# Performance work log

Measured on AMD Instinct MI355X. Metric: run time of the kernel, lower is better.

The kernel has to match this reference:

```python
import jax, jax.numpy as jnp
import numpy as np

LABEL_LEN = 48
PRED_LEN = 96
D_MODEL = 512


def _pos_embed(L, d):
    pos = np.arange(L, dtype=np.float32)[:, None]
    div = np.exp(np.arange(0, d, 2, dtype=np.float32) * (-np.log(10000.0) / d))
    pe = np.zeros((L, d), np.float32)
    pe[:, 0::2] = np.sin(pos * div)
    pe[:, 1::2] = np.cos(pos * div)
    return jnp.asarray(pe)


def _embed(x, conv_w):
    # x: [B, L, C]; circular conv1d k=3 (TokenEmbedding) + sinusoidal PE
    xp = jnp.pad(jnp.transpose(x, (0, 2, 1)), ((0, 0), (0, 0), (1, 1)), mode='wrap')
    y = jax.lax.conv_general_dilated(xp, conv_w, (1,), 'VALID',
                                     dimension_numbers=('NCH', 'OIH', 'NCH'))
    y = jnp.transpose(y, (0, 2, 1))  # [B, L, D]
    return y + _pos_embed(y.shape[1], y.shape[2])


def _lstm_cell(x, h, c, Wih, Whh, b):
    g = x @ Wih.T + h @ Whh.T + b
    i, f, gg, o = jnp.split(g, 4, axis=-1)  # torch gate order i,f,g,o
    c = jax.nn.sigmoid(f) * c + jax.nn.sigmoid(i) * jnp.tanh(gg)
    h = jax.nn.sigmoid(o) * jnp.tanh(c)
    return h, c


def _lstm(xs, Wih, Whh, b):
    B, _, _ = xs.shape
    H = Whh.shape[1]
    init = (jnp.zeros((B, H), xs.dtype), jnp.zeros((B, H), xs.dtype))
    def step(carry, x):
        h, c = _lstm_cell(x, carry[0], carry[1], Wih, Whh, b)
        return (h, c), h
    (h, c), ys = jax.lax.scan(step, init, jnp.transpose(xs, (1, 0, 2)))
    return jnp.transpose(ys, (1, 0, 2)), h, c


def _forward(x_enc, x_dec, emb_enc_w, emb_dec_w, enc_Wih, enc_Whh, enc_b,
             dec_Wih, dec_Whh, dec_b, attn_W, attn_b, v, fc_W, fc_b,
             proj_W, proj_b):
    H = D_MODEL
    enc_in = _embed(x_enc, emb_enc_w)                 # [B, Le, H]
    dec_in = _embed(x_dec, emb_dec_w)                 # [B, Ld, H]
    enc_out, h0, c0 = _lstm(enc_in, enc_Wih, enc_Whh, enc_b)  # [B, Le, H]

    # precompute encoder part of Bahdanau score: attn(cat(h, enc)) splits columnwise
    Wh, We = attn_W[:, :H], attn_W[:, H:]
    enc_part = jnp.einsum('blh,kh->blk', enc_out, We) + attn_b   # [B, Le, H]
    # precompute input gates for decoded timesteps
    xs = dec_in[:, LABEL_LEN:PRED_LEN, :]                         # [B, T, H]
    xg = jnp.einsum('bth,gh->btg', xs, dec_Wih) + dec_b           # [B, T, 4H]

    def step(carry, xg_t):
        h, c = carry
        g = xg_t + h @ dec_Whh.T
        i, f, gg, o = jnp.split(g, 4, axis=-1)
        c = jax.nn.sigmoid(f) * c + jax.nn.sigmoid(i) * jnp.tanh(gg)
        h = jax.nn.sigmoid(o) * jnp.tanh(c)
        feat = jnp.tanh(enc_part + (h @ Wh.T)[:, None, :])        # [B, Le, H]
        scores = feat @ v                                          # [B, Le]
        aw = jax.nn.softmax(scores, axis=1)
        ctx = jnp.einsum('bl,blh->bh', aw, enc_out)                # [B, H]
        out = jnp.concatenate([h, ctx], axis=-1) @ fc_W.T + fc_b   # [B, H]
        return (h, c), out

    (_, _), outs = jax.lax.scan(step, (h0, c0), jnp.transpose(xg, (1, 0, 2)))
    outs = jnp.transpose(outs, (1, 0, 2))                          # [B, T, H]
    proj = outs @ proj_W.T + proj_b                                # [B, T, c_out]
    # forward slices [:, -pred_len:, :]; T = pred_len-label_len < pred_len -> identity
    return proj


def setup_inputs() -> dict:
    key = jax.random.key(0)
    ks = jax.random.split(key, 20)
    s = 0.05
    H = D_MODEL
    return {
        'x_enc': jax.random.normal(ks[0], (64, 512, 7), jnp.float32),
        'x_dec': jax.random.normal(ks[1], (64, 144, 7), jnp.float32),
        'emb_enc_w': jax.random.normal(ks[2], (H, 7, 3), jnp.float32) * s,
        'emb_dec_w': jax.random.normal(ks[3], (H, 7, 3), jnp.float32) * s,
        'enc_Wih': jax.random.normal(ks[4], (4 * H, H), jnp.float32) * s,
        'enc_Whh': jax.random.normal(ks[5], (4 * H, H), jnp.float32) * s,
        'enc_b': jax.random.normal(ks[6], (4 * H,), jnp.float32) * s,
        'dec_Wih': jax.random.normal(ks[7], (4 * H, H), jnp.float32) * s,
        'dec_Whh': jax.random.normal(ks[8], (4 * H, H), jnp.float32) * s,
        'dec_b': jax.random.normal(ks[9], (4 * H,), jnp.float32) * s,
        'attn_W': jax.random.normal(ks[10], (H, 2 * H), jnp.float32) * s,
        'attn_b': jax.random.normal(ks[11], (H,), jnp.float32) * s,
        'v': jax.random.uniform(ks[12], (H,), jnp.float32),
        'fc_W': jax.random.normal(ks[13], (H, 2 * H), jnp.float32) * s,
        'fc_b': jax.random.normal(ks[14], (H,), jnp.float32) * s,
        'proj_W': jax.random.normal(ks[15], (7, H), jnp.float32) * s,
        'proj_b': jax.random.normal(ks[16], (7,), jnp.float32) * s,
    }


def reference(x_enc, x_dec, emb_enc_w, emb_dec_w, enc_Wih, enc_Whh, enc_b,
              dec_Wih, dec_Whh, dec_b, attn_W, attn_b, v, fc_W, fc_b,
              proj_W, proj_b):
    return _forward(x_enc, x_dec, emb_enc_w, emb_dec_w, enc_Wih, enc_Whh,
                    enc_b, dec_Wih, dec_Whh, dec_b, attn_W, attn_b, v,
                    fc_W, fc_b, proj_W, proj_b)
```

## Files before the change

kernel.cpp:

```cpp
#include <hip/hip_runtime.h>
#include <hip/hip_bf16.h>


typedef short bf16x8 __attribute__((ext_vector_type(8)));
typedef float f32x4 __attribute__((ext_vector_type(4)));

static __device__ __forceinline__ float bf2f(unsigned short u){
  return __uint_as_float(((unsigned)u) << 16);
}
static __device__ __forceinline__ unsigned short f2bf(float f){
  unsigned x = __float_as_uint(f);
  return (unsigned short)((x + 0x7fffu + ((x >> 16) & 1u)) >> 16);
}
static __device__ __forceinline__ float sigm(float x){
  return __builtin_amdgcn_rcpf(1.f + __builtin_amdgcn_exp2f(-1.44269504f*x));
}
static __device__ __forceinline__ float tanh2(float x){
  return 1.f - 2.f*__builtin_amdgcn_rcpf(1.f + __builtin_amdgcn_exp2f(2.88539008f*x));
}

static __device__ __forceinline__ unsigned ldu(const unsigned* p){
  return __hip_atomic_load(p, __ATOMIC_RELAXED, __HIP_MEMORY_SCOPE_AGENT);
}
static __device__ __forceinline__ void stu(unsigned* p, unsigned v){
  __hip_atomic_store(p, v, __ATOMIC_RELAXED, __HIP_MEMORY_SCOPE_AGENT);
}
static __device__ __forceinline__ unsigned long long ldq(const unsigned long long* p){
  return __hip_atomic_load(p, __ATOMIC_RELAXED, __HIP_MEMORY_SCOPE_AGENT);
}
static __device__ __forceinline__ void stq(unsigned long long* p, unsigned long long v){
  __hip_atomic_store(p, v, __ATOMIC_RELAXED, __HIP_MEMORY_SCOPE_AGENT);
}
#define VMWAIT() __asm__ __volatile__("s_waitcnt vmcnt(0)" ::: "memory")


__global__ void cast_k(const float* __restrict__ src, unsigned short* __restrict__ dst, int n){
  int i = blockIdx.x*256 + threadIdx.x;
  if (i < n) dst[i] = f2bf(src[i]);
}

__global__ void split_attn_k(const float* __restrict__ aw,
                             unsigned short* __restrict__ wh, unsigned short* __restrict__ we){
  int i = blockIdx.x*256 + threadIdx.x;
  int nrow = i >> 9, k = i & 511;
  wh[i] = f2bf(aw[(size_t)nrow*1024 + k]);
  we[i] = f2bf(aw[(size_t)nrow*1024 + 512 + k]);
}

__global__ __launch_bounds__(512) void embed_k(const float* __restrict__ x,
    const float* __restrict__ wconv, unsigned short* __restrict__ out,
    int Bsz, int Lx, int l0, int lcount, int mode){
  __shared__ float wl[512*21];
  __shared__ float xl[66*7];
  int nch = (lcount + 63) / 64;
  int b = blockIdx.x / nch, ci = blockIdx.x % nch;
  int tid = threadIdx.x;
  for (int i = tid; i < 512*21; i += 512) wl[i] = wconv[i];
  int lstart = l0 + ci*64;
  int cnt = l0 + lcount - lstart; if (cnt > 64) cnt = 64;
  int nwin = (cnt + 2) * 7;
  for (int i = tid; i < nwin; i += 512){
    int wr = i / 7, c = i % 7;
    int gl = lstart - 1 + wr;
    gl = (gl + Lx) % Lx;
    xl[i] = x[((size_t)b*Lx + gl)*7 + c];
  }
  __syncthreads();
  int o = tid;
  float fe = (float)(o & ~1);
  float div = __expf(fe * -0.0179889461f);
  const float* wrow = &wl[o*21];
  for (int li = 0; li < cnt; ++li){
    int l = lstart + li;
    float acc = 0.f;
    #pragma unroll
    for (int c = 0; c < 7; ++c)
      #pragma unroll
      for (int kk = 0; kk < 3; ++kk)
        acc += xl[(li + kk)*7 + c] * wrow[c*3 + kk];
    float arg = (float)l * div;
    acc += (o & 1) ? cosf(arg) : sinf(arg);
    size_t oi = mode ? (((size_t)b*lcount + (l - l0))*512 + o)
                     : (((size_t)l*Bsz + b)*512 + o);
    out[oi] = f2bf(acc);
  }
}

__global__ __launch_bounds__(256) void gemm_nt(const unsigned short* __restrict__ A, int lda,
    const unsigned short* __restrict__ Bw, int ldb, const float* __restrict__ bias,
    unsigned short* __restrict__ C, int ldc, int M, int N, int K){
  __shared__ __align__(16) unsigned short Asm[128*40];
  __shared__ __align__(16) unsigned short Bsm[128*40];
  const int tid = threadIdx.x;
  const int m0 = blockIdx.y * 128, n0 = blockIdx.x * 128;
  const int lane = tid & 63;
  const int wid = tid >> 6;
  const int wm = (wid >> 1) * 64, wn = (wid & 1) * 64;
  const int fr = lane & 15, q = lane >> 4;
  f32x4 acc[4][4];
  #pragma unroll
  for (int i=0;i<4;i++)
    #pragma unroll
    for(int j=0;j<4;j++) acc[i][j] = (f32x4){0.f,0.f,0.f,0.f};
  for (int k0 = 0; k0 < K; k0 += 32){
    #pragma unroll
    for (int c = 0; c < 2; ++c){
      int ch = tid + c*256;
      int r = ch >> 2, s = (ch & 3) * 8;
      *(uint4*)&Asm[r*40 + s] = *(const uint4*)&A[(size_t)(m0 + r)*lda + k0 + s];
      *(uint4*)&Bsm[r*40 + s] = *(const uint4*)&Bw[(size_t)(n0 + r)*ldb + k0 + s];
    }
    __syncthreads();
    bf16x8 af[4], bfv[4];
    #pragma unroll
    for (int i=0;i<4;i++){
      af[i]  = *(const bf16x8*)&Asm[(wm + i*16 + fr)*40 + q*8];
      bfv[i] = *(const bf16x8*)&Bsm[(wn + i*16 + fr)*40 + q*8];
    }
    #pragma unroll
    for (int i=0;i<4;i++)
      #pragma unroll
      for (int j=0;j<4;j++)
        acc[i][j] = __builtin_amdgcn_mfma_f32_16x16x32_bf16(af[i], bfv[j], acc[i][j], 0,0,0);
    __syncthreads();
  }
  #pragma unroll
  for (int i=0;i<4;i++){
    #pragma unroll
    for (int j=0;j<4;j++){
      int n = n0 + wn + j*16 + fr;
      float bv = bias ? bias[n] : 0.f;
      #pragma unroll
      for (int r=0;r<4;r++){
        int m = m0 + wm + i*16 + q*4 + r;
        C[(size_t)m*ldc + n] = f2bf(acc[i][j][r] + bv);
      }
    }
  }
}

__global__ __launch_bounds__(256) void gemm_ntf(const unsigned short* __restrict__ A, int lda,
    const unsigned short* __restrict__ Bw, int ldb,
    float* __restrict__ C, int ldc, int M, int N, int K){
  __shared__ __align__(16) unsigned short Asm[128*40];
  __shared__ __align__(16) unsigned short Bsm[128*40];
  const int tid = threadIdx.x;
  const int m0 = blockIdx.y * 128, n0 = blockIdx.x * 128;
  const int lane = tid & 63;
  const int wid = tid >> 6;
  const int wm = (wid >> 1) * 64, wn = (wid & 1) * 64;
  const int fr = lane & 15, q = lane >> 4;
  f32x4 acc[4][4];
  #pragma unroll
  for (int i=0;i<4;i++)
    #pragma unroll
    for(int j=0;j<4;j++) acc[i][j] = (f32x4){0.f,0.f,0.f,0.f};
  for (int k0 = 0; k0 < K; k0 += 32){
    #pragma unroll
    for (int c = 0; c < 2; ++c){
      int ch = tid + c*256;
      int r = ch >> 2, s = (ch & 3) * 8;
      *(uint4*)&Asm[r*40 + s] = *(const uint4*)&A[(size_t)(m0 + r)*lda + k0 + s];
      *(uint4*)&Bsm[r*40 + s] = *(const uint4*)&Bw[(size_t)(n0 + r)*ldb + k0 + s];
    }
    __syncthreads();
    bf16x8 af[4], bfv[4];
    #pragma unroll
    for (int i=0;i<4;i++){
      af[i]  = *(const bf16x8*)&Asm[(wm + i*16 + fr)*40 + q*8];
      bfv[i] = *(const bf16x8*)&Bsm[(wn + i*16 + fr)*40 + q*8];
    }
    #pragma unroll
    for (int i=0;i<4;i++)
      #pragma unroll
      for (int j=0;j<4;j++)
        acc[i][j] = __builtin_amdgcn_mfma_f32_16x16x32_bf16(af[i], bfv[j], acc[i][j], 0,0,0);
    __syncthreads();
  }
  #pragma unroll
  for (int i=0;i<4;i++){
    #pragma unroll
    for (int j=0;j<4;j++){
      int n = n0 + wn + j*16 + fr;
      #pragma unroll
      for (int r=0;r<4;r++){
        int m = m0 + wm + i*16 + q*4 + r;
        C[(size_t)m*ldc + n] = acc[i][j][r];
      }
    }
  }
}

__global__ __launch_bounds__(512) void lstm_enc(
    const unsigned short* __restrict__ xw,
    const unsigned short* __restrict__ whh,
    float* __restrict__ cbuf, unsigned long long* __restrict__ hbuf,
    unsigned short* __restrict__ encout,
    int t0, int nsteps, unsigned* __restrict__ slots){
  __shared__ __align__(16) unsigned short wlds[128*516];
  __shared__ __align__(16) unsigned short hblds[16*516];
  __shared__ float gbufE[256*9];
  const int tid = threadIdx.x;
  const int g = blockIdx.x & 7, j = blockIdx.x >> 3;
  const int b0 = g*8, u0 = j*64;
  for (int idx = tid; idx < 128*64; idx += 512){
    int n = idx >> 6, ch = idx & 63;
    int R = (n >> 6)*512 + u0 + (n & 63);
    *(uint4*)&wlds[n*516 + ch*8] = *(const uint4*)&whh[(size_t)R*512 + ch*8];
  }
  for (int idx = tid; idx < 1032; idx += 512)
    *(unsigned long long*)&hblds[8*516 + idx*4] = 0ull;
  const int lane = tid & 63, wv = tid >> 6, fr = lane & 15, q = lane >> 4;
  const int m = tid >> 6, j2 = tid & 63;
  bf16x8 breg[16];
  {
    int rl = 128 + wv*16 + fr;
    int R2 = (rl >> 6)*512 + u0 + (rl & 63);
    const unsigned short* wp2 = &whh[(size_t)R2*512 + q*8];
    #pragma unroll
    for (int kk = 0; kk < 16; ++kk)
      breg[kk] = *(const bf16x8*)&wp2[kk*32];
  }
  float cst = cbuf[(b0 + m)*512 + u0 + j2];
  unsigned* myslot = slots + g*16 + j;
  const unsigned* gslots = slots + g*16;
  unsigned short px0, px1, px2, px3;
  {
    size_t xi = ((size_t)t0*64 + b0 + m)*2048 + u0 + j2;
    px0 = xw[xi]; px1 = xw[xi + 512]; px2 = xw[xi + 1024]; px3 = xw[xi + 1536];
  }
  __syncthreads();
  for (int s = 0; s < nsteps; ++s){
    const int t = t0 + s;
    const int rp = t & 1, wp = rp ^ 1;
    {
      const unsigned long long* hq = hbuf + (size_t)rp*8192 + (size_t)b0*128;
      unsigned long long v0 = ldq(&hq[tid]);
      unsigned long long v1 = ldq(&hq[tid + 512]);
      int b2 = tid >> 7, q2 = tid & 127;
      *(unsigned long long*)&hblds[b2*516 + q2*4] = v0;
      *(unsigned long long*)&hblds[(b2 + 4)*516 + q2*4] = v1;
    }
    __syncthreads();
    f32x4 acc = {0.f,0.f,0.f,0.f}, acc2 = {0.f,0.f,0.f,0.f};
    #pragma unroll
    for (int kk = 0; kk < 16; ++kk){
      bf16x8 av = *(const bf16x8*)&hblds[fr*516 + kk*32 + q*8];
      bf16x8 bv = *(const bf16x8*)&wlds[(wv*16 + fr)*516 + kk*32 + q*8];
      acc  = __builtin_amdgcn_mfma_f32_16x16x32_bf16(av, bv,       acc,  0,0,0);
      acc2 = __builtin_amdgcn_mfma_f32_16x16x32_bf16(av, breg[kk], acc2, 0,0,0);
    }
    if (q < 2){
      #pragma unroll
      for (int r = 0; r < 4; ++r){
        gbufE[(wv*16 + fr)*9 + q*4 + r] = acc[r];
        gbufE[(128 + wv*16 + fr)*9 + q*4 + r] = acc2[r];
      }
    }
    __syncthreads();
    unsigned short hv;
    {
      float gi = gbufE[(j2)*9 + m]        + bf2f(px0);
      float gf = gbufE[(64 + j2)*9 + m]   + bf2f(px1);
      float gg = gbufE[(128 + j2)*9 + m]  + bf2f(px2);
      float go = gbufE[(192 + j2)*9 + m]  + bf2f(px3);
      float cc = sigm(gf)*cst + sigm(gi)*tanh2(gg);
      float hh = sigm(go)*tanh2(cc);
      cst = cc;
      hv = f2bf(hh);
      unsigned other = (unsigned)__shfl_xor((int)(unsigned)hv, 1);
      unsigned pair = ((unsigned)hv) | (other << 16);
      unsigned pair2 = (unsigned)__shfl_xor((int)pair, 2);
      if ((j2 & 3) == 0){
        unsigned long long qw = (((unsigned long long)pair2) << 32) | (unsigned long long)pair;
        stq(&hbuf[(size_t)wp*8192 + (size_t)(b0+m)*128 + ((u0 + j2) >> 2)], qw);
      }
    }
    VMWAIT();
    __syncthreads();
    if (tid == 0) stu(myslot, (unsigned)(t + 1));
    encout[((size_t)(b0+m)*512 + t)*512 + u0 + j2] = hv;
    if (s == nsteps - 1) cbuf[(b0+m)*512 + u0 + j2] = cst;
    else {
      size_t xi = ((size_t)(t+1)*64 + b0 + m)*2048 + u0 + j2;
      px0 = xw[xi]; px1 = xw[xi + 512]; px2 = xw[xi + 1024]; px3 = xw[xi + 1536];
    }
    if (tid < 64){
      unsigned target = (unsigned)(t + 1);
      bool mine = (tid < 8);
      const unsigned* sp = gslots + (tid & 7);
      while (true){
        bool ok = true;
        if (mine) ok = (ldu(sp) >= target);
        if (__all(ok)) break;
        __builtin_amdgcn_s_sleep(1);
      }
    }
    __syncthreads();
  }
}

__global__ __launch_bounds__(512) void dec_h(
    const unsigned short* __restrict__ xg,
    const unsigned short* __restrict__ whh,
    const float* __restrict__ cbuf, unsigned long long* __restrict__ hbuf,
    unsigned short* __restrict__ X,
    unsigned* __restrict__ slots){
  __shared__ __align__(16) unsigned short wlds[128*516];
  __shared__ __align__(16) unsigned short hblds[16*516];
  __shared__ float gbufE[256*9];
  const int tid = threadIdx.x;
  const int g = blockIdx.x & 7, j = blockIdx.x >> 3;
  const int b0 = g*8, u0 = j*64;
  for (int idx = tid; idx < 128*64; idx += 512){
    int n = idx >> 6, ch = idx & 63;
    int R = (n >> 6)*512 + u0 + (n & 63);
    *(uint4*)&wlds[n*516 + ch*8] = *(const uint4*)&whh[(size_t)R*512 + ch*8];
  }
  for (int idx = tid; idx < 1032; idx += 512)
    *(unsigned long long*)&hblds[8*516 + idx*4] = 0ull;
  const int lane = tid & 63, wv = tid >> 6, fr = lane & 15, q = lane >> 4;
  const int m = tid >> 6, j2 = tid & 63;
  bf16x8 breg[16];
  {
    int rl = 128 + wv*16 + fr;
    int R2 = (rl >> 6)*512 + u0 + (rl & 63);
    const unsigned short* wp2 = &whh[(size_t)R2*512 + q*8];
    #pragma unroll
    for (int kk = 0; kk < 16; ++kk)
      breg[kk] = *(const bf16x8*)&wp2[kk*32];
  }
  float cst = cbuf[(b0 + m)*512 + u0 + j2];
  unsigned* myslot = slots + g*16 + j;
  const unsigned* gslots = slots + g*16;
  unsigned short px0, px1, px2, px3;
  {
    size_t xi = ((size_t)(b0 + m)*48)*2048 + u0 + j2;
    px0 = xg[xi]; px1 = xg[xi + 512]; px2 = xg[xi + 1024]; px3 = xg[xi + 1536];
  }
  __syncthreads();
  for (int t = 0; t < 48; ++t){
    const int rp = t & 1, wp = rp ^ 1;
    {
      const unsigned long long* hq = hbuf + (size_t)rp*8192 + (size_t)b0*128;
      unsigned long long v0 = ldq(&hq[tid]);
      unsigned long long v1 = ldq(&hq[tid + 512]);
      int b2 = tid >> 7, q2 = tid & 127;
      *(unsigned long long*)&hblds[b2*516 + q2*4] = v0;
      *(unsigned long long*)&hblds[(b2 + 4)*516 + q2*4] = v1;
    }
    __syncthreads();
    f32x4 acc = {0.f,0.f,0.f,0.f}, acc2 = {0.f,0.f,0.f,0.f};
    #pragma unroll
    for (int kk = 0; kk < 16; ++kk){
      bf16x8 av = *(const bf16x8*)&hblds[fr*516 + kk*32 + q*8];
      bf16x8 bv = *(const bf16x8*)&wlds[(wv*16 + fr)*516 + kk*32 + q*8];
      acc  = __builtin_amdgcn_mfma_f32_16x16x32_bf16(av, bv,       acc,  0,0,0);
      acc2 = __builtin_amdgcn_mfma_f32_16x16x32_bf16(av, breg[kk], acc2, 0,0,0);
    }
    if (q < 2){
      #pragma unroll
      for (int r = 0; r < 4; ++r){
        gbufE[(wv*16 + fr)*9 + q*4 + r] = acc[r];
        gbufE[(128 + wv*16 + fr)*9 + q*4 + r] = acc2[r];
      }
    }
    __syncthreads();
    unsigned short hv;
    {
      float gi = gbufE[(j2)*9 + m]        + bf2f(px0);
      float gf = gbufE[(64 + j2)*9 + m]   + bf2f(px1);
      float gg = gbufE[(128 + j2)*9 + m]  + bf2f(px2);
      float go = gbufE[(192 + j2)*9 + m]  + bf2f(px3);
      float cc = sigm(gf)*cst + sigm(gi)*tanh2(gg);
      float hh = sigm(go)*tanh2(cc);
      cst = cc;
      hv = f2bf(hh);
      unsigned other = (unsigned)__shfl_xor((int)(unsigned)hv, 1);
      unsigned pair = ((unsigned)hv) | (other << 16);
      unsigned pair2 = (unsigned)__shfl_xor((int)pair, 2);
      if ((j2 & 3) == 0){
        unsigned long long qw = (((unsigned long long)pair2) << 32) | (unsigned long long)pair;
        stq(&hbuf[(size_t)wp*8192 + (size_t)(b0+m)*128 + ((u0 + j2) >> 2)], qw);
      }
    }
    VMWAIT();
    __syncthreads();
    if (tid == 0) stu(myslot, (unsigned)(t + 1));
    X[((size_t)t*64 + b0 + m)*1024 + u0 + j2] = hv;
    if (t < 47){
      size_t xi = ((size_t)(b0 + m)*48 + t + 1)*2048 + u0 + j2;
      px0 = xg[xi]; px1 = xg[xi + 512]; px2 = xg[xi + 1024]; px3 = xg[xi + 1536];
    }
    if (tid < 64){
      unsigned target = (unsigned)(t + 1);
      bool mine = (tid < 8);
      const unsigned* sp = gslots + (tid & 7);
      while (true){
        bool ok = true;
        if (mine) ok = (ldu(sp) >= target);
        if (__all(ok)) break;
        __builtin_amdgcn_s_sleep(1);
      }
    }
    __syncthreads();
  }
}

__global__ __launch_bounds__(256) void attn_scores(
    const unsigned short* __restrict__ encpart,
    const float* __restrict__ hwh,
    const float* __restrict__ vvec,
    float* __restrict__ scores){
  __shared__ __align__(16) float hwhs[512];
  __shared__ __align__(16) float vm2s[512];
  __shared__ float red[4];
  const int tid = threadIdx.x;
  const int b = blockIdx.x >> 3, lc = blockIdx.x & 7;
  const int l = tid >> 2, kq = tid & 3;
  const int lane = tid & 63, wv = tid >> 6;
  vm2s[tid] = -2.f * vvec[tid];
  vm2s[tid+256] = -2.f * vvec[tid+256];
  __syncthreads();
  float vsumf;
  {
    float x = vm2s[tid] + vm2s[tid+256];
    #pragma unroll
    for (int off=32; off; off>>=1) x += __shfl_xor(x, off);
    if (lane == 0) red[wv] = x;
    __syncthreads();
    vsumf = -0.5f * (red[0]+red[1]+red[2]+red[3]);
  }
  bf16x8 epr[16];
  {
    const unsigned short* ep = encpart + ((size_t)(b*512 + lc*64 + l))*512 + kq*128;
    #pragma unroll
    for (int i = 0; i < 16; ++i) epr[i] = *(const bf16x8*)&ep[i*8];
  }
  const float C = 2.88539008f;
  for (int t = 0; t < 48; ++t){
    __syncthreads();
    hwhs[tid]     = C * hwh[((size_t)t*64 + b)*512 + tid];
    hwhs[tid+256] = C * hwh[((size_t)t*64 + b)*512 + tid + 256];
    __syncthreads();
    float sacc = 0.f;
    #pragma unroll
    for (int kk = 0; kk < 16; ++kk){
      float4 h0 = *(const float4*)&hwhs[kq*128 + kk*8];
      float4 h1 = *(const float4*)&hwhs[kq*128 + kk*8 + 4];
      float4 v0 = *(const float4*)&vm2s[kq*128 + kk*8];
      float4 v1 = *(const float4*)&vm2s[kq*128 + kk*8 + 4];
      const unsigned short* e = (const unsigned short*)&epr[kk];
      float hw[8] = {h0.x,h0.y,h0.z,h0.w,h1.x,h1.y,h1.z,h1.w};
      float vv[8] = {v0.x,v0.y,v0.z,v0.w,v1.x,v1.y,v1.z,v1.w};
      #pragma unroll
      for (int ee = 0; ee < 8; ++ee){
        float a = fmaf(bf2f(e[ee]), C, hw[ee]);
        sacc = fmaf(vv[ee], __builtin_amdgcn_rcpf(1.f + __builtin_amdgcn_exp2f(a)), sacc);
      }
    }
    sacc += __shfl_xor(sacc, 1);
    sacc += __shfl_xor(sacc, 2);
    if (kq == 0) scores[((size_t)t*64 + b)*512 + lc*64 + l] = vsumf + sacc;
  }
}

__global__ __launch_bounds__(256) void softmax_aw(
    const float* __restrict__ scores, unsigned short* __restrict__ awb){
  __shared__ float red[4];
  const int row = blockIdx.x, tid = threadIdx.x;
  const int lane = tid & 63, wv = tid >> 6;
  float v0 = scores[(size_t)row*512 + tid];
  float v1 = scores[(size_t)row*512 + tid + 256];
  float mx = fmaxf(v0, v1);
  #pragma unroll
  for (int off=32; off; off>>=1) mx = fmaxf(mx, __shfl_xor(mx, off));
  if (lane == 0) red[wv] = mx;
  __syncthreads();
  mx = fmaxf(fmaxf(red[0],red[1]), fmaxf(red[2],red[3]));
  __syncthreads();
  float e0 = __expf(v0 - mx), e1 = __expf(v1 - mx);
  float ps = e0 + e1;
  #pragma unroll
  for (int off=32; off; off>>=1) ps += __shfl_xor(ps, off);
  if (lane == 0) red[wv] = ps;
  __syncthreads();
  float inv = 1.f / (red[0]+red[1]+red[2]+red[3]);
  awb[(size_t)row*512 + tid]       = f2bf(e0 * inv);
  awb[(size_t)row*512 + tid + 256] = f2bf(e1 * inv);
}

__global__ __launch_bounds__(256) void ctx_k(
    const unsigned short* __restrict__ awb,
    const unsigned short* __restrict__ encout,
    unsigned short* __restrict__ X){
  __shared__ unsigned short awt[512*12];
  const int tid = threadIdx.x;
  const int b = blockIdx.x >> 2, t0 = (blockIdx.x & 3)*12;
  for (int i = tid; i < 12*256; i += 256){
    int tt = i >> 8, d = i & 255;
    unsigned u = *(const unsigned*)&awb[((size_t)(t0+tt)*64 + b)*512 + d*2];
    awt[(2*d)*12 + tt]   = (unsigned short)(u & 0xffffu);
    awt[(2*d+1)*12 + tt] = (unsigned short)(u >> 16);
  }
  __syncthreads();
  float a0[12], a1[12];
  #pragma unroll
  for (int j = 0; j < 12; ++j){ a0[j] = 0.f; a1[j] = 0.f; }
  const unsigned* eo = (const unsigned*)(encout + (size_t)b*512*512) + tid;
  for (int ll = 0; ll < 512; ++ll){
    unsigned ee = eo[(size_t)ll*256];
    float e0 = __uint_as_float((ee & 0xffffu) << 16);
    float e1 = __uint_as_float(ee & 0xffff0000u);
    const unsigned* wp2 = (const unsigned*)&awt[ll*12];
    float w[12];
    #pragma unroll
    for (int z = 0; z < 6; ++z){
      unsigned wu = wp2[z];
      w[2*z]   = bf2f((unsigned short)(wu & 0xffffu));
      w[2*z+1] = bf2f((unsigned short)(wu >> 16));
    }
    #pragma unroll
    for (int j = 0; j < 12; ++j){
      a0[j] = fmaf(w[j], e0, a0[j]);
      a1[j] = fmaf(w[j], e1, a1[j]);
    }
  }
  #pragma unroll
  for (int j = 0; j < 12; ++j){
    size_t r = (size_t)(t0+j)*64 + b;
    unsigned pk = ((unsigned)f2bf(a0[j])) | (((unsigned)f2bf(a1[j])) << 16);
    *(unsigned*)&X[r*1024 + 512 + 2*tid] = pk;
  }
}

__global__ void proj_k(const unsigned short* __restrict__ outs,
                       const float* __restrict__ pw, const float* __restrict__ pb,
                       float* __restrict__ out){
  int gid = blockIdx.x*256 + threadIdx.x;
  if (gid >= 64*48*7) return;
  int r = gid / 7, oc = gid % 7;
  int b = r & 63, t = r >> 6;
  const unsigned short* orow = outs + (size_t)r*512;
  const float* wrow = pw + oc*512;
  float s = pb[oc];
  for (int k = 0; k < 512; k += 8){
    bf16x8 o8 = *(const bf16x8*)&orow[k];
    #pragma unroll
    for (int e=0;e<8;e++) s += bf2f(((unsigned short*)&o8)[e]) * wrow[k+e];
  }
  out[((size_t)b*48 + t)*7 + oc] = s;
}

extern "C" void kernel_launch(void* const* d_in, const int* in_sizes, int n_in,
                              void* d_out, int out_size, void* d_ws, size_t ws_size,
                              hipStream_t stream){
  (void)in_sizes; (void)n_in; (void)out_size; (void)ws_size;
  const float* x_enc   = (const float*)d_in[0];
  const float* x_dec   = (const float*)d_in[1];
  const float* w_emb_e = (const float*)d_in[2];
  const float* w_emb_d = (const float*)d_in[3];
  const float* enc_Wih = (const float*)d_in[4];
  const float* enc_Whh = (const float*)d_in[5];
  const float* enc_b   = (const float*)d_in[6];
  const float* dec_Wih = (const float*)d_in[7];
  const float* dec_Whh = (const float*)d_in[8];
  const float* dec_b   = (const float*)d_in[9];
  const float* attn_W  = (const float*)d_in[10];
  const float* attn_b  = (const float*)d_in[11];
  const float* vvec    = (const float*)d_in[12];
  const float* fc_W    = (const float*)d_in[13];
  const float* fc_b    = (const float*)d_in[14];
  const float* proj_W  = (const float*)d_in[15];
  const float* proj_b  = (const float*)d_in[16];
  float* out = (float*)d_out;

  char* ws = (char*)d_ws;
  size_t off = 0;
  auto alloc = [&](size_t bytes)->char*{
    char* p = ws + off;
    off = (off + bytes + 255) & ~(size_t)255;
    return p;
  };
  unsigned short* encxw  = (unsigned short*)alloc(512ull*64*2048*2);
  unsigned short* encin  = (unsigned short*)alloc(512ull*64*512*2);
  unsigned short* encout = (unsigned short*)alloc(64ull*512*512*2);
  unsigned short* xs     = (unsigned short*)alloc(64ull*48*512*2);
  unsigned short* xg     = (unsigned short*)alloc(64ull*48*2048*2);
  unsigned short* Xb     = (unsigned short*)alloc(3072ull*1024*2);
  float* hwh    = (float*)alloc(3072ull*512*4);
  float* scores = (float*)alloc(3072ull*512*4);
  unsigned short* awb    = (unsigned short*)alloc(3072ull*512*2);
  unsigned short* outsb  = (unsigned short*)alloc(3072ull*512*2);
  unsigned short* wih_e  = (unsigned short*)alloc(2048ull*512*2);
  unsigned short* whh_e  = (unsigned short*)alloc(2048ull*512*2);
  unsigned short* wih_d  = (unsigned short*)alloc(2048ull*512*2);
  unsigned short* whh_d  = (unsigned short*)alloc(2048ull*512*2);
  unsigned short* whq    = (unsigned short*)alloc(512ull*512*2);
  unsigned short* weq    = (unsigned short*)alloc(512ull*512*2);
  unsigned short* fcw    = (unsigned short*)alloc(512ull*1024*2);
  unsigned long long* hbuf = (unsigned long long*)alloc(2ull*64*128*8);
  float* cbuf   = (float*)alloc(64ull*512*4);
  unsigned* eslots = (unsigned*)alloc(4*64*4);
  unsigned* dslots = (unsigned*)alloc(4*64*4);

  hipMemsetAsync(hbuf, 0, 2ull*64*128*8, stream);
  hipMemsetAsync(cbuf, 0, 64ull*512*4, stream);
  hipMemsetAsync(eslots, 0, 4*64*4, stream);
  hipMemsetAsync(dslots, 0, 4*64*4, stream);

  cast_k<<<4096, 256, 0, stream>>>(enc_Wih, wih_e, 2048*512);
  cast_k<<<4096, 256, 0, stream>>>(enc_Whh, whh_e, 2048*512);
  cast_k<<<4096, 256, 0, stream>>>(dec_Wih, wih_d, 2048*512);
  cast_k<<<4096, 256, 0, stream>>>(dec_Whh, whh_d, 2048*512);
  cast_k<<<2048, 256, 0, stream>>>(fc_W, fcw, 512*1024);
  split_attn_k<<<1024, 256, 0, stream>>>(attn_W, whq, weq);

  embed_k<<<512, 512, 0, stream>>>(x_enc, w_emb_e, encin, 64, 512, 0, 512, 0);
  embed_k<<<64, 512, 0, stream>>>(x_dec, w_emb_d, xs, 64, 144, 48, 48, 1);

  gemm_nt<<<dim3(16, 24), 256, 0, stream>>>(xs, 512, wih_d, 512, dec_b, xg, 2048, 3072, 2048, 512);

  gemm_nt<<<dim3(16, 256), 256, 0, stream>>>(encin, 512, wih_e, 512, enc_b, encxw, 2048, 32768, 2048, 512);
  lstm_enc<<<64, 512, 0, stream>>>(encxw, whh_e, cbuf, hbuf, encout, 0, 512, eslots);

  gemm_nt<<<dim3(4, 256), 256, 0, stream>>>(encout, 512, weq, 512, attn_b, encin, 512, 32768, 512, 512);

  dec_h<<<64, 512, 0, stream>>>(xg, whh_d, cbuf, hbuf, Xb, dslots);

  gemm_ntf<<<dim3(4, 24), 256, 0, stream>>>(Xb, 1024, whq, 512, hwh, 512, 3072, 512, 512);

  attn_scores<<<512, 256, 0, stream>>>(encin , hwh, vvec, scores);
  softmax_aw<<<3072, 256, 0, stream>>>(scores, awb);
  ctx_k<<<256, 256, 0, stream>>>(awb, encout, Xb);

  gemm_nt<<<dim3(4, 24), 256, 0, stream>>>(Xb, 1024, fcw, 1024, fc_b, outsb, 512, 3072, 512, 1024);

  proj_k<<<84, 256, 0, stream>>>(outsb, proj_W, proj_b, out);
}
```

Measured before the change: 2.280 ms.

## Replace slot-counter barrier with tagged per-element h exchange in LSTM kernels

The persistent LSTM encoder and decoder kernels no longer publish h through packed 64-bit stores followed by a vmcnt wait, a block barrier and a per-block slot counter that peers spin on. Each hidden value is now stored as a 32-bit word carrying its bf16 value and a 16-bit step tag, written with a release store. Readers poll only the foreign slices until the tag matches, and the block's own slice is written straight into LDS. This removes a barrier and a separate flag round-trip from each of the serial recurrence steps, at the cost of doubling the size of the h exchange buffer and issuing more, smaller polling loads.

```diff
diff --git a/kernel.cpp b/kernel.cpp
--- a/kernel.cpp
+++ b/kernel.cpp
@@ -22,16 +22,9 @@
 static __device__ __forceinline__ unsigned ldu(const unsigned* p){
   return __hip_atomic_load(p, __ATOMIC_RELAXED, __HIP_MEMORY_SCOPE_AGENT);
 }
-static __device__ __forceinline__ void stu(unsigned* p, unsigned v){
-  __hip_atomic_store(p, v, __ATOMIC_RELAXED, __HIP_MEMORY_SCOPE_AGENT);
-}
-static __device__ __forceinline__ unsigned long long ldq(const unsigned long long* p){
-  return __hip_atomic_load(p, __ATOMIC_RELAXED, __HIP_MEMORY_SCOPE_AGENT);
-}
-static __device__ __forceinline__ void stq(unsigned long long* p, unsigned long long v){
-  __hip_atomic_store(p, v, __ATOMIC_RELAXED, __HIP_MEMORY_SCOPE_AGENT);
-}
-#define VMWAIT() __asm__ __volatile__("s_waitcnt vmcnt(0)" ::: "memory")
+static __device__ __forceinline__ void st_rel(unsigned* p, unsigned v){
+  __hip_atomic_store(p, v, __ATOMIC_RELEASE, __HIP_MEMORY_SCOPE_AGENT);
+}
 
 
 __global__ void cast_k(const float* __restrict__ src, unsigned short* __restrict__ dst, int n){
@@ -194,9 +187,9 @@
 __global__ __launch_bounds__(512) void lstm_enc(
     const unsigned short* __restrict__ xw,
     const unsigned short* __restrict__ whh,
-    float* __restrict__ cbuf, unsigned long long* __restrict__ hbuf,
+    float* __restrict__ cbuf, unsigned* __restrict__ hbuf,
     unsigned short* __restrict__ encout,
-    int t0, int nsteps, unsigned* __restrict__ slots){
+    int t0, int nsteps){
   __shared__ __align__(16) unsigned short wlds[128*516];
   __shared__ __align__(16) unsigned short hblds[16*516];
   __shared__ float gbufE[256*9];
@@ -222,8 +215,6 @@
       breg[kk] = *(const bf16x8*)&wp2[kk*32];
   }
   float cst = cbuf[(b0 + m)*512 + u0 + j2];
-  unsigned* myslot = slots + g*16 + j;
-  const unsigned* gslots = slots + g*16;
   unsigned short px0, px1, px2, px3;
   {
     size_t xi = ((size_t)t0*64 + b0 + m)*2048 + u0 + j2;
@@ -232,14 +223,26 @@
   __syncthreads();
   for (int s = 0; s < nsteps; ++s){
     const int t = t0 + s;
-    const int rp = t & 1, wp = rp ^ 1;
+    const unsigned rtag = (unsigned)t & 0xffffu, wtag = (unsigned)(t + 1) & 0xffffu;
+    const int rp = t & 1, wp = (t + 1) & 1;
     {
-      const unsigned long long* hq = hbuf + (size_t)rp*8192 + (size_t)b0*128;
-      unsigned long long v0 = ldq(&hq[tid]);
-      unsigned long long v1 = ldq(&hq[tid + 512]);
-      int b2 = tid >> 7, q2 = tid & 127;
-      *(unsigned long long*)&hblds[b2*516 + q2*4] = v0;
-      *(unsigned long long*)&hblds[(b2 + 4)*516 + q2*4] = v1;
+      const int b2 = tid >> 6, c0 = tid & 63;
+      const unsigned* base = hbuf + (size_t)rp*32768 + (size_t)(b0 + b2)*512 + c0;
+      unsigned need = (s == 0) ? 0xffu : (0xffu & ~(1u << j));
+      unsigned vals[8] = {0,0,0,0,0,0,0,0};
+      while (need){
+        #pragma unroll
+        for (int i = 0; i < 8; ++i){
+          if (need & (1u << i)){
+            unsigned x = ldu(base + i*64);
+            if ((x & 0xffffu) == rtag){ vals[i] = x; need &= ~(1u << i); }
+          }
+        }
+        if (need) __builtin_amdgcn_s_sleep(1);
+      }
+      #pragma unroll
+      for (int i = 0; i < 8; ++i)
+        if (i != j || s == 0) hblds[b2*516 + c0 + i*64] = (unsigned short)(vals[i] >> 16);
     }
     __syncthreads();
     f32x4 acc = {0.f,0.f,0.f,0.f}, acc2 = {0.f,0.f,0.f,0.f};
@@ -268,44 +271,25 @@
       float hh = sigm(go)*tanh2(cc);
       cst = cc;
       hv = f2bf(hh);
-      unsigned other = (unsigned)__shfl_xor((int)(unsigned)hv, 1);
-      unsigned pair = ((unsigned)hv) | (other << 16);
-      unsigned pair2 = (unsigned)__shfl_xor((int)pair, 2);
-      if ((j2 & 3) == 0){
-        unsigned long long qw = (((unsigned long long)pair2) << 32) | (unsigned long long)pair;
-        stq(&hbuf[(size_t)wp*8192 + (size_t)(b0+m)*128 + ((u0 + j2) >> 2)], qw);
-      }
-    }
-    VMWAIT();
-    __syncthreads();
-    if (tid == 0) stu(myslot, (unsigned)(t + 1));
+      hblds[m*516 + u0 + j2] = hv;
+      st_rel(&hbuf[(size_t)wp*32768 + (size_t)(b0 + m)*512 + u0 + j2],
+             (((unsigned)hv) << 16) | wtag);
+    }
     encout[((size_t)(b0+m)*512 + t)*512 + u0 + j2] = hv;
     if (s == nsteps - 1) cbuf[(b0+m)*512 + u0 + j2] = cst;
     else {
       size_t xi = ((size_t)(t+1)*64 + b0 + m)*2048 + u0 + j2;
       px0 = xw[xi]; px1 = xw[xi + 512]; px2 = xw[xi + 1024]; px3 = xw[xi + 1536];
     }
-    if (tid < 64){
-      unsigned target = (unsigned)(t + 1);
-      bool mine = (tid < 8);
-      const unsigned* sp = gslots + (tid & 7);
-      while (true){
-        bool ok = true;
-        if (mine) ok = (ldu(sp) >= target);
-        if (__all(ok)) break;
-        __builtin_amdgcn_s_sleep(1);
-      }
-    }
-    __syncthreads();
   }
 }
 
 __global__ __launch_bounds__(512) void dec_h(
     const unsigned short* __restrict__ xg,
     const unsigned short* __restrict__ whh,
-    const float* __restrict__ cbuf, unsigned long long* __restrict__ hbuf,
+    const float* __restrict__ cbuf, unsigned* __restrict__ hbuf,
     unsigned short* __restrict__ X,
-    unsigned* __restrict__ slots){
+    int tagbase){
   __shared__ __align__(16) unsigned short wlds[128*516];
   __shared__ __align__(16) unsigned short hblds[16*516];
   __shared__ float gbufE[256*9];
@@ -331,8 +315,6 @@
       breg[kk] = *(const bf16x8*)&wp2[kk*32];
   }
   float cst = cbuf[(b0 + m)*512 + u0 + j2];
-  unsigned* myslot = slots + g*16 + j;
-  const unsigned* gslots = slots + g*16;
   unsigned short px0, px1, px2, px3;
   {
     size_t xi = ((size_t)(b0 + m)*48)*2048 + u0 + j2;
@@ -340,14 +322,27 @@
   }
   __syncthreads();
   for (int t = 0; t < 48; ++t){
-    const int rp = t & 1, wp = rp ^ 1;
+    const int S = tagbase + t;
+    const unsigned rtag = (unsigned)S & 0xffffu, wtag = (unsigned)(S + 1) & 0xffffu;
+    const int rp = S & 1, wp = (S + 1) & 1;
     {
-      const unsigned long long* hq = hbuf + (size_t)rp*8192 + (size_t)b0*128;
-      unsigned long long v0 = ldq(&hq[tid]);
-      unsigned long long v1 = ldq(&hq[tid + 512]);
-      int b2 = tid >> 7, q2 = tid & 127;
-      *(unsigned long long*)&hblds[b2*516 + q2*4] = v0;
-      *(unsigned long long*)&hblds[(b2 + 4)*516 + q2*4] = v1;
+      const int b2 = tid >> 6, c0 = tid & 63;
+      const unsigned* base = hbuf + (size_t)rp*32768 + (size_t)(b0 + b2)*512 + c0;
+      unsigned need = (t == 0) ? 0xffu : (0xffu & ~(1u << j));
+      unsigned vals[8] = {0,0,0,0,0,0,0,0};
+      while (need){
+        #pragma unroll
+        for (int i = 0; i < 8; ++i){
+          if (need & (1u << i)){
+            unsigned x = ldu(base + i*64);
+            if ((x & 0xffffu) == rtag){ vals[i] = x; need &= ~(1u << i); }
+          }
+        }
+        if (need) __builtin_amdgcn_s_sleep(1);
+      }
+      #pragma unroll
+      for (int i = 0; i < 8; ++i)
+        if (i != j || t == 0) hblds[b2*516 + c0 + i*64] = (unsigned short)(vals[i] >> 16);
     }
     __syncthreads();
     f32x4 acc = {0.f,0.f,0.f,0.f}, acc2 = {0.f,0.f,0.f,0.f};
@@ -376,34 +371,15 @@
       float hh = sigm(go)*tanh2(cc);
       cst = cc;
       hv = f2bf(hh);
-      unsigned other = (unsigned)__shfl_xor((int)(unsigned)hv, 1);
-      unsigned pair = ((unsigned)hv) | (other << 16);
-      unsigned pair2 = (unsigned)__shfl_xor((int)pair, 2);
-      if ((j2 & 3) == 0){
-        unsigned long long qw = (((unsigned long long)pair2) << 32) | (unsigned long long)pair;
-        stq(&hbuf[(size_t)wp*8192 + (size_t)(b0+m)*128 + ((u0 + j2) >> 2)], qw);
-      }
-    }
-    VMWAIT();
-    __syncthreads();
-    if (tid == 0) stu(myslot, (unsigned)(t + 1));
+      hblds[m*516 + u0 + j2] = hv;
+      st_rel(&hbuf[(size_t)wp*32768 + (size_t)(b0 + m)*512 + u0 + j2],
+             (((unsigned)hv) << 16) | wtag);
+    }
     X[((size_t)t*64 + b0 + m)*1024 + u0 + j2] = hv;
     if (t < 47){
       size_t xi = ((size_t)(b0 + m)*48 + t + 1)*2048 + u0 + j2;
       px0 = xg[xi]; px1 = xg[xi + 512]; px2 = xg[xi + 1024]; px3 = xg[xi + 1536];
     }
-    if (tid < 64){
-      unsigned target = (unsigned)(t + 1);
-      bool mine = (tid < 8);
-      const unsigned* sp = gslots + (tid & 7);
-      while (true){
-        bool ok = true;
-        if (mine) ok = (ldu(sp) >= target);
-        if (__all(ok)) break;
-        __builtin_amdgcn_s_sleep(1);
-      }
-    }
-    __syncthreads();
   }
 }
 
@@ -599,15 +575,11 @@
   unsigned short* whq    = (unsigned short*)alloc(512ull*512*2);
   unsigned short* weq    = (unsigned short*)alloc(512ull*512*2);
   unsigned short* fcw    = (unsigned short*)alloc(512ull*1024*2);
-  unsigned long long* hbuf = (unsigned long long*)alloc(2ull*64*128*8);
+  unsigned* hbuf = (unsigned*)alloc(2ull*64*512*4);
   float* cbuf   = (float*)alloc(64ull*512*4);
-  unsigned* eslots = (unsigned*)alloc(4*64*4);
-  unsigned* dslots = (unsigned*)alloc(4*64*4);
-
-  hipMemsetAsync(hbuf, 0, 2ull*64*128*8, stream);
+
+  hipMemsetAsync(hbuf, 0, 2ull*64*512*4, stream);
   hipMemsetAsync(cbuf, 0, 64ull*512*4, stream);
-  hipMemsetAsync(eslots, 0, 4*64*4, stream);
-  hipMemsetAsync(dslots, 0, 4*64*4, stream);
 
   cast_k<<<4096, 256, 0, stream>>>(enc_Wih, wih_e, 2048*512);
   cast_k<<<4096, 256, 0, stream>>>(enc_Whh, whh_e, 2048*512);
@@ -622,11 +594,11 @@
   gemm_nt<<<dim3(16, 24), 256, 0, stream>>>(xs, 512, wih_d, 512, dec_b, xg, 2048, 3072, 2048, 512);
 
   gemm_nt<<<dim3(16, 256), 256, 0, stream>>>(encin, 512, wih_e, 512, enc_b, encxw, 2048, 32768, 2048, 512);
-  lstm_enc<<<64, 512, 0, stream>>>(encxw, whh_e, cbuf, hbuf, encout, 0, 512, eslots);
+  lstm_enc<<<64, 512, 0, stream>>>(encxw, whh_e, cbuf, hbuf, encout, 0, 512);
 
   gemm_nt<<<dim3(4, 256), 256, 0, stream>>>(encout, 512, weq, 512, attn_b, encin, 512, 32768, 512, 512);
 
-  dec_h<<<64, 512, 0, stream>>>(xg, whh_d, cbuf, hbuf, Xb, dslots);
+  dec_h<<<64, 512, 0, stream>>>(xg, whh_d, cbuf, hbuf, Xb, 512);
 
   gemm_ntf<<<dim3(4, 24), 256, 0, stream>>>(Xb, 1024, whq, 512, hwh, 512, 3072, 512, 512);
 
```

After: 5.691 ms. 2.5x slower.
